# Kernel tuning notes

Hardware: AMD Instinct MI355X
Metric: run time of the kernel (lower is better)

The kernel has to match this reference:

```python
import jax, jax.numpy as jnp
import numpy as np

DIM = 256
CTX_DIM = 768
GROUPS = 8
EPS = 1e-5


def setup_inputs() -> dict:
    key = jax.random.key(0)
    ks = jax.random.split(key, 16)
    B, C, H, W, L = 16, DIM, 64, 64, 77
    s_conv = 1.0 / np.sqrt(C * 9)
    s_q = 1.0 / np.sqrt(C)
    s_kv = 1.0 / np.sqrt(CTX_DIM)
    return {
        "x": jax.random.normal(ks[0], (B, C, H, W), jnp.float32),
        "context": jax.random.normal(ks[1], (B, L, CTX_DIM), jnp.float32),
        "conv_w": jax.random.uniform(ks[2], (C, C, 3, 3), jnp.float32, -s_conv, s_conv),
        "conv_b": jax.random.uniform(ks[3], (C,), jnp.float32, -s_conv, s_conv),
        "gn_w": jnp.ones((C,), jnp.float32),
        "gn_b": jnp.zeros((C,), jnp.float32),
        "wq": jax.random.uniform(ks[4], (C, C), jnp.float32, -s_q, s_q),
        "bq": jax.random.uniform(ks[5], (C,), jnp.float32, -s_q, s_q),
        "wk": jax.random.uniform(ks[6], (C, CTX_DIM), jnp.float32, -s_kv, s_kv),
        "bk": jax.random.uniform(ks[7], (C,), jnp.float32, -s_kv, s_kv),
        "wv": jax.random.uniform(ks[8], (C, CTX_DIM), jnp.float32, -s_kv, s_kv),
        "bv": jax.random.uniform(ks[9], (C,), jnp.float32, -s_kv, s_kv),
        "wo": jax.random.uniform(ks[10], (C, C), jnp.float32, -s_q, s_q),
        "bo": jax.random.uniform(ks[11], (C,), jnp.float32, -s_q, s_q),
    }


def _group_norm(h, gn_w, gn_b):
    B, C, H, W = h.shape
    g = h.reshape(B, GROUPS, C // GROUPS, H, W)
    mean = g.mean(axis=(2, 3, 4), keepdims=True)
    var = g.var(axis=(2, 3, 4), keepdims=True)
    g = (g - mean) * jax.lax.rsqrt(var + EPS)
    h = g.reshape(B, C, H, W)
    return h * gn_w[None, :, None, None] + gn_b[None, :, None, None]


def reference(x, context, conv_w, conv_b, gn_w, gn_b, wq, bq, wk, bk, wv, bv, wo, bo):
    B, C, H, W = x.shape
    # conv 3x3, padding=1 (NCHW, OIHW)
    h = jax.lax.conv_general_dilated(
        x, conv_w, window_strides=(1, 1), padding=((1, 1), (1, 1)),
        dimension_numbers=("NCHW", "OIHW", "NCHW"))
    h = h + conv_b[None, :, None, None]
    h = jax.nn.silu(_group_norm(h, gn_w, gn_b))
    # flatten spatial -> tokens: [B, HW, C]
    hf = h.reshape(B, C, H * W).transpose(0, 2, 1)
    q = hf @ wq.T + bq                     # [B, HW, C]
    k = context @ wk.T + bk                # [B, L, C]
    v = context @ wv.T + bv                # [B, L, C]
    scale = 1.0 / jnp.sqrt(jnp.asarray(C, q.dtype))
    att = jax.nn.softmax(jnp.einsum("bqc,bkc->bqk", q, k) * scale, axis=-1)
    o = jnp.einsum("bqk,bkc->bqc", att, v) @ wo.T + bo
    h_att = o.transpose(0, 2, 1).reshape(B, C, H, W)
    return x + h_att
```

## Files before the change

### kernel.cpp

```cpp
#include <hip/hip_runtime.h>
#include <stdint.h>

#define B_  16
#define C_  256
#define HW_ 4096
#define Hp  66
#define PP  4356
#define EPS_ 1e-5f

typedef unsigned short u16;
typedef unsigned int   u32;
typedef __attribute__((ext_vector_type(4))) float  f32x4;
typedef __attribute__((ext_vector_type(8))) __bf16 bf16x8;
typedef __attribute__((ext_vector_type(8))) u16    u16x8;

__device__ __forceinline__ float bf2f(u16 u){ u32 x = ((u32)u)<<16; float f; __builtin_memcpy(&f,&x,4); return f; }
__device__ __forceinline__ u16 f2bf(float f){ u32 x; __builtin_memcpy(&x,&f,4); u32 r = x + 0x7fffu + ((x>>16)&1u); return (u16)(r>>16); }

__device__ __forceinline__ void g2l16(const void* g, void* l){
  __builtin_amdgcn_global_load_lds((__attribute__((address_space(1))) void*)(void*)g,
                                   (__attribute__((address_space(3))) void*)l, 16, 0, 0);
}
__device__ __forceinline__ bf16x8 ldfrag(const u16* p){
  u16x8 r = *(const u16x8*)p;
  return __builtin_bit_cast(bf16x8, r);
}

__global__ __launch_bounds__(256) void k_pad(const float* __restrict__ x, u16* __restrict__ xpT){
  int bid = blockIdx.x; int b = bid/66, hh = bid - b*66; int tid = threadIdx.x;
  u16* rowbase = xpT + (size_t)(b*PP + hh*Hp)*C_;
  if(hh==0 || hh==65){
    u32* p = (u32*)rowbase;
    for(int i=tid;i<66*C_/2;i+=256) p[i]=0u;
    return;
  }
  if(tid<128) ((u32*)rowbase)[tid]=0u;
  else ((u32*)(rowbase + 65*C_))[tid-128]=0u;
  int h = hh-1;
  __shared__ float Lt[64*65];
  for(int cc=0; cc<4; cc++){
    int c0=cc*64;
    int ci = tid>>2, w0 = (tid&3)*16;
    const float* xs = x + ((size_t)(b*C_ + c0+ci)*HW_) + h*64 + w0;
    for(int j=0;j<4;j++){
      float4 v = *(const float4*)(xs + j*4);
      Lt[ci*65 + w0 + j*4 + 0] = v.x;
      Lt[ci*65 + w0 + j*4 + 1] = v.y;
      Lt[ci*65 + w0 + j*4 + 2] = v.z;
      Lt[ci*65 + w0 + j*4 + 3] = v.w;
    }
    __syncthreads();
    int w = tid>>2, cj = (tid&3)*16;
    union { u16 u[16]; uint4 v[2]; } outu;
    for(int j=0;j<16;j++) outu.u[j] = f2bf(Lt[(cj+j)*65 + w]);
    uint4* dst = (uint4*)(rowbase + (size_t)(w+1)*C_ + c0 + cj);
    dst[0]=outu.v[0]; dst[1]=outu.v[1];
    __syncthreads();
  }
}

__global__ __launch_bounds__(256) void k_repack(
    const float* __restrict__ conv_w, const float* __restrict__ wq, const float* __restrict__ wo,
    const float* __restrict__ wk, const float* __restrict__ wv, const float* __restrict__ ctx,
    u16* __restrict__ wBt, u16* __restrict__ wqB, u16* __restrict__ woB,
    u16* __restrict__ wkvB, u16* __restrict__ ctxB, float* __restrict__ stats){
  int i = blockIdx.x*256 + threadIdx.x;
  if(i < 589824){ int co = i/2304, k = i - co*2304; int t = k>>8, ci = k&255;
    wBt[i] = f2bf(conv_w[(co*256+ci)*9 + t]); return; }
  i -= 589824;
  if(i < 65536){ wqB[i] = f2bf(wq[i]); return; } i -= 65536;
  if(i < 65536){ woB[i] = f2bf(wo[i]); return; } i -= 65536;
  if(i < 196608){ wkvB[i] = f2bf(wk[i]); return; } i -= 196608;
  if(i < 196608){ wkvB[196608+i] = f2bf(wv[i]); return; } i -= 196608;
  if(i < 946176){ ctxB[i] = f2bf(ctx[i]); return; } i -= 946176;
  if(i < 512){ stats[i] = 0.f; }
}

__global__ __launch_bounds__(256, 2) void k_conv(const u16* __restrict__ xpT, const u16* __restrict__ wBt,
    const float* __restrict__ conv_b, u16* __restrict__ h, float* __restrict__ stats){
  __shared__ u16 As[264*32];
  __shared__ u16 Bs[256*32];
  int bid = blockIdx.x;
  int b = bid >> 5, hp = bid & 31;
  int tid = threadIdx.x;
  int w = tid>>6, lane = tid&63, ln = lane&15, qd = lane>>4;
  int wm = w&1, wn = w>>1;
  const u16* Abase = xpT + (size_t)(b*PP + hp*132)*C_;
  f32x4 acc[4][8] = {};
  int hr_[4], wp_[4];
  #pragma unroll
  for(int mf=0;mf<4;mf++){ int p = wm*64 + mf*16 + ln; hr_[mf] = p>>6; wp_[mf] = p&63; }

  for(int ci=0; ci<8; ci++){
    int ci0 = ci*32;
    #pragma unroll
    for(int r=0;r<5;r++){
      int c = r*256 + tid;
      if(c < 1056){
        int ipix = c>>2, atom = c&3;
        g2l16(Abase + (size_t)ipix*C_ + ci0 + atom*8, &As[c*8]);
      }
    }
    for(int t=0;t<9;t++){
      int dy = (t*11)>>5, dx = t - dy*3;
      #pragma unroll
      for(int r=0;r<4;r++){
        int c = r*256 + tid;
        int co = c>>2, atom = c&3;
        g2l16(wBt + (size_t)co*2304 + t*256 + ci0 + atom*8, &Bs[c*8]);
      }
      __syncthreads();
      bf16x8 af[4], bfv[8];
      #pragma unroll
      for(int mf=0;mf<4;mf++){
        int ipix = (hr_[mf]+dy)*66 + wp_[mf] + dx;
        af[mf] = ldfrag(&As[ipix*32 + qd*8]);
      }
      #pragma unroll
      for(int nf=0;nf<8;nf++) bfv[nf] = ldfrag(&Bs[(wn*128+nf*16+ln)*32 + qd*8]);
      #pragma unroll
      for(int mf=0;mf<4;mf++)
        #pragma unroll
        for(int nf=0;nf<8;nf++)
          acc[mf][nf] = __builtin_amdgcn_mfma_f32_16x16x32_bf16(af[mf], bfv[nf], acc[mf][nf], 0,0,0);
      __syncthreads();
    }
  }
  float s[4]={0,0,0,0}, q[4]={0,0,0,0};
  int p0 = hp*128;
  for(int nf=0;nf<8;nf++){
    int n = wn*128 + nf*16 + ln;
    float bias = conv_b[n];
    for(int mf=0;mf<4;mf++){
      for(int r=0;r<4;r++){
        int p = wm*64 + mf*16 + qd*4 + r;
        float v = acc[mf][nf][r] + bias;
        h[((size_t)(b*HW_ + p0 + p))*C_ + n] = f2bf(v);
        s[nf>>1]+=v; q[nf>>1]+=v*v;
      }
    }
  }
  for(int off=32;off>=1;off>>=1){
    #pragma unroll
    for(int g=0;g<4;g++){ s[g]+=__shfl_down(s[g],off,64); q[g]+=__shfl_down(q[g],off,64); }
  }
  if(lane==0){
    #pragma unroll
    for(int g=0;g<4;g++){
      atomicAdd(&stats[(b*8 + wn*4 + g)*2+0], s[g]);
      atomicAdd(&stats[(b*8 + wn*4 + g)*2+1], q[g]);
    }
  }
}

__global__ __launch_bounds__(256) void k_gnsilu(u16* __restrict__ hbuf, const float* __restrict__ stats,
      const float* __restrict__ gnw, const float* __restrict__ gnb){
  size_t i = ((size_t)blockIdx.x*256 + threadIdx.x)*4;
  int c0 = (int)(i & 255);
  size_t row = i >> 8;
  int b = (int)(row >> 12);
  int g = c0 >> 5;
  float sm = stats[(b*8+g)*2], qm = stats[(b*8+g)*2+1];
  float mean = sm*(1.f/131072.f);
  float var  = qm*(1.f/131072.f) - mean*mean;
  float rstd = rsqrtf(var + EPS_);
  u32* p = (u32*)(hbuf + i);
  u32 v0 = p[0], v1 = p[1];
  u16 in[4] = {(u16)(v0&0xffff),(u16)(v0>>16),(u16)(v1&0xffff),(u16)(v1>>16)};
  u16 outv[4];
  for(int j=0;j<4;j++){
    float v = bf2f(in[j]);
    v = (v-mean)*rstd*gnw[c0+j] + gnb[c0+j];
    float s = v/(1.f+__expf(-v));
    outv[j] = f2bf(s);
  }
  p[0] = (u32)outv[0] | ((u32)outv[1]<<16);
  p[1] = (u32)outv[2] | ((u32)outv[3]<<16);
}

__global__ __launch_bounds__(256) void k_qproj(const u16* __restrict__ hf, const u16* __restrict__ wqB,
    const float* __restrict__ bq, u16* __restrict__ qb){
  __shared__ u16 As[128*32];
  __shared__ u16 Bs[128*32];
  int bid = blockIdx.x;
  int nt = bid & 1, mt = bid >> 1;
  int co0 = nt*128;
  int tid = threadIdx.x;
  int w=tid>>6, lane=tid&63, ln=lane&15, qd=lane>>4, wm=w>>1, wn=w&1;
  int srow=tid>>2, koff=(tid&3)*8;
  f32x4 acc[4][4] = {};
  for(int kt=0;kt<8;kt++){
    for(int j=0;j<2;j++){
      int m = srow + j*64;
      g2l16(hf  + ((size_t)(mt*128+m)*256 + kt*32 + koff), &As[(size_t)tid*8 + j*2048]);
      g2l16(wqB + ((size_t)(co0+m)*256 + kt*32 + koff),    &Bs[(size_t)tid*8 + j*2048]);
    }
    __syncthreads();
    bf16x8 af[4], bfv[4];
    for(int mf=0;mf<4;mf++) af[mf]=ldfrag(&As[(wm*64+mf*16+ln)*32+qd*8]);
    for(int nf=0;nf<4;nf++) bfv[nf]=ldfrag(&Bs[(wn*64+nf*16+ln)*32+qd*8]);
    for(int mf=0;mf<4;mf++) for(int nf=0;nf<4;nf++)
      acc[mf][nf]=__builtin_amdgcn_mfma_f32_16x16x32_bf16(af[mf],bfv[nf],acc[mf][nf],0,0,0);
    __syncthreads();
  }
  for(int mf=0;mf<4;mf++) for(int nf=0;nf<4;nf++){
    int nl=wn*64+nf*16+ln; float bias=bq[co0+nl];
    for(int r=0;r<4;r++){
      int ml=wm*64+mf*16+qd*4+r;
      qb[((size_t)(mt*128+ml))*256 + co0+nl] = f2bf(acc[mf][nf][r]+bias);
    }
  }
}

__global__ __launch_bounds__(256) void k_kvproj(const u16* __restrict__ ctxB, const u16* __restrict__ wkvB,
    const float* __restrict__ bk, const float* __restrict__ bv,
    u16* __restrict__ kb, u16* __restrict__ vT){
  __shared__ u16 As[64*128];
  __shared__ u16 Bs[64*128];
  int bid = blockIdx.x;
  int nt = bid & 7, mt = bid >> 3;
  int n0 = nt*64, m0 = mt*64;
  int tid=threadIdx.x, w=tid>>6, lane=tid&63, ln=lane&15, qd=lane>>4;
  int wm = w&1, wn = w>>1;
  f32x4 acc[2][2]={};
  for(int kt=0;kt<6;kt++){
    #pragma unroll
    for(int r=0;r<4;r++){
      int c = r*256 + tid;
      int row = c>>4, atom = c&15;
      g2l16(ctxB + ((size_t)(m0+row)*768 + kt*128 + atom*8), &As[c*8]);
      g2l16(wkvB + ((size_t)(n0+row)*768 + kt*128 + atom*8), &Bs[c*8]);
    }
    __syncthreads();
    #pragma unroll
    for(int kk=0;kk<4;kk++){
      bf16x8 af[2], bfv[2];
      #pragma unroll
      for(int mf=0;mf<2;mf++) af[mf]=ldfrag(&As[(wm*32+mf*16+ln)*128 + kk*32 + qd*8]);
      #pragma unroll
      for(int nf=0;nf<2;nf++) bfv[nf]=ldfrag(&Bs[(wn*32+nf*16+ln)*128 + kk*32 + qd*8]);
      #pragma unroll
      for(int mf=0;mf<2;mf++)
        #pragma unroll
        for(int nf=0;nf<2;nf++)
          acc[mf][nf]=__builtin_amdgcn_mfma_f32_16x16x32_bf16(af[mf],bfv[nf],acc[mf][nf],0,0,0);
    }
    __syncthreads();
  }
  for(int mf=0;mf<2;mf++) for(int nf=0;nf<2;nf++){
    int ng = n0 + wn*32 + nf*16 + ln;
    float bias = ng<256 ? bk[ng] : bv[ng-256];
    for(int r=0;r<4;r++){
      int mg = m0 + wm*32 + mf*16 + qd*4 + r;
      if(mg<1232){
        float v=acc[mf][nf][r]+bias;
        int bb=mg/77, l=mg-bb*77;
        if(ng<256) kb[((size_t)(bb*77+l))*256+ng]=f2bf(v);
        else vT[((size_t)(bb*256+(ng-256)))*96 + l]=f2bf(v);
      }
    }
  }
}

__global__ __launch_bounds__(256) void k_attn(const u16* __restrict__ qg, const u16* __restrict__ kb,
    const u16* __restrict__ vT, u16* __restrict__ ob){
  __shared__ u16 Qs[4096];
  __shared__ u16 KVs[4096];
  __shared__ u16 Sb[128*84];
  __shared__ u16 Pb[128*104];
  int bid=blockIdx.x; int b=bid>>5, qt=bid&31; int p0=qt*128;
  int tid=threadIdx.x, w=tid>>6, lane=tid&63, ln=lane&15, qd=lane>>4;
  int srow=tid>>2, koff=(tid&3)*8;
  f32x4 Sa[2][5]={};
  for(int kt=0;kt<8;kt++){
    for(int j=0;j<2;j++){
      int m=srow+j*64;
      g2l16(qg + ((size_t)(b*HW_+p0+m)*256 + kt*32+koff), &Qs[(size_t)tid*8+j*2048]);
    }
    for(int j=0;j<2;j++){
      int cja = tid + j*256;
      if(cja < 320){
        int l = cja>>2, ko2=(cja&3)*8;
        g2l16(kb + ((size_t)(b*77+l)*256 + kt*32+ko2), &KVs[(size_t)cja*8]);
      }
    }
    __syncthreads();
    bf16x8 af[2], bfv[5];
    for(int mf=0;mf<2;mf++) af[mf]=ldfrag(&Qs[(w*32+mf*16+ln)*32+qd*8]);
    for(int nf=0;nf<5;nf++) bfv[nf]=ldfrag(&KVs[(nf*16+ln)*32+qd*8]);
    for(int mf=0;mf<2;mf++) for(int nf=0;nf<5;nf++)
      Sa[mf][nf]=__builtin_amdgcn_mfma_f32_16x16x32_bf16(af[mf],bfv[nf],Sa[mf][nf],0,0,0);
    __syncthreads();
  }
  for(int mf=0;mf<2;mf++) for(int nf=0;nf<5;nf++) for(int r=0;r<4;r++){
    int ml=w*32+mf*16+qd*4+r, nl=nf*16+ln;
    Sb[ml*84+nl]=f2bf(Sa[mf][nf][r]*0.0625f);
  }
  __syncthreads();
  if(tid<128){
    const u16* srp = &Sb[tid*84];
    u16* prow = &Pb[tid*104];
    float mx=-1e30f;
    for(int j2=0;j2<77;j2++){ float v=bf2f(srp[j2]); mx=fmaxf(mx,v); }
    float sum=0.f;
    for(int j2=0;j2<77;j2++){ float e=__expf(bf2f(srp[j2])-mx); sum+=e; prow[j2]=f2bf(e); }
    float inv=1.f/sum;
    for(int j2=0;j2<77;j2++){ prow[j2]=f2bf(bf2f(prow[j2])*inv); }
    for(int j2=77;j2<104;j2++) prow[j2]=0;
  }
  __syncthreads();
  for(int nh=0;nh<2;nh++){
    f32x4 Oa[2][8]={};
    for(int kt2=0;kt2<3;kt2++){
      for(int j=0;j<2;j++){
        int chunk=tid+j*256;
        int co=chunk>>2, ko2=(chunk&3)*8;
        g2l16(vT + ((size_t)(b*256+nh*128+co)*96 + kt2*32+ko2), &KVs[(size_t)chunk*8]);
      }
      __syncthreads();
      bf16x8 af[2], bfv[8];
      for(int mf=0;mf<2;mf++) af[mf]=ldfrag(&Pb[(w*32+mf*16+ln)*104 + kt2*32+qd*8]);
      for(int nf=0;nf<8;nf++) bfv[nf]=ldfrag(&KVs[(nf*16+ln)*32+qd*8]);
      for(int mf=0;mf<2;mf++) for(int nf=0;nf<8;nf++)
        Oa[mf][nf]=__builtin_amdgcn_mfma_f32_16x16x32_bf16(af[mf],bfv[nf],Oa[mf][nf],0,0,0);
      __syncthreads();
    }
    for(int mf=0;mf<2;mf++) for(int nf=0;nf<8;nf++) for(int r=0;r<4;r++){
      int ml=w*32+mf*16+qd*4+r, nl=nh*128+nf*16+ln;
      ob[((size_t)(b*HW_+p0+ml))*256+nl]=f2bf(Oa[mf][nf][r]);
    }
  }
}

__global__ __launch_bounds__(256) void k_oproj(const u16* __restrict__ ob, const u16* __restrict__ woB,
    const float* __restrict__ bo, const float* __restrict__ x, float* __restrict__ outp){
  __shared__ u16 As[128*32];
  __shared__ u16 Bs[128*32];
  int bid=blockIdx.x;
  int b=bid>>6; int rr=bid&63; int cm=rr>>5, pt=rr&31;
  int c0=cm*128, p0=pt*128;
  int tid=threadIdx.x, w=tid>>6, lane=tid&63, ln=lane&15, qd=lane>>4, wm=w>>1, wn=w&1;
  int srow=tid>>2, koff=(tid&3)*8;
  f32x4 acc[4][4]={};
  for(int kt=0;kt<8;kt++){
    for(int j=0;j<2;j++){
      int m=srow+j*64;
      g2l16(woB + ((size_t)(c0+m)*256 + kt*32+koff),        &As[(size_t)tid*8+j*2048]);
      g2l16(ob  + ((size_t)(b*HW_+p0+m)*256 + kt*32+koff),  &Bs[(size_t)tid*8+j*2048]);
    }
    __syncthreads();
    bf16x8 af[4], bfv[4];
    for(int mf=0;mf<4;mf++) af[mf]=ldfrag(&As[(wm*64+mf*16+ln)*32+qd*8]);
    for(int nf=0;nf<4;nf++) bfv[nf]=ldfrag(&Bs[(wn*64+nf*16+ln)*32+qd*8]);
    for(int mf=0;mf<4;mf++) for(int nf=0;nf<4;nf++)
      acc[mf][nf]=__builtin_amdgcn_mfma_f32_16x16x32_bf16(af[mf],bfv[nf],acc[mf][nf],0,0,0);
    __syncthreads();
  }
  for(int mf=0;mf<4;mf++) for(int r=0;r<4;r++){
    int cl=c0+wm*64+mf*16+qd*4+r;
    float bias=bo[cl];
    for(int nf=0;nf<4;nf++){
      int pl=p0+wn*64+nf*16+ln;
      size_t idx=((size_t)(b*C_+cl))*HW_+pl;
      outp[idx]=x[idx]+acc[mf][nf][r]+bias;
    }
  }
}

extern "C" void kernel_launch(void* const* d_in, const int* in_sizes, int n_in,
                              void* d_out, int out_size, void* d_ws, size_t ws_size,
                              hipStream_t stream){
  const float* x      = (const float*)d_in[0];
  const float* ctx    = (const float*)d_in[1];
  const float* conv_w = (const float*)d_in[2];
  const float* conv_b = (const float*)d_in[3];
  const float* gnw    = (const float*)d_in[4];
  const float* gnb    = (const float*)d_in[5];
  const float* wq     = (const float*)d_in[6];
  const float* bq     = (const float*)d_in[7];
  const float* wk     = (const float*)d_in[8];
  const float* bk     = (const float*)d_in[9];
  const float* wv     = (const float*)d_in[10];
  const float* bv     = (const float*)d_in[11];
  const float* wo     = (const float*)d_in[12];
  const float* bo     = (const float*)d_in[13];
  char* ws = (char*)d_ws;
  u16* xpT  = (u16*)(ws + 0);
  u16* wBt  = (u16*)(ws + 35684352);
  u16* wqB  = (u16*)(ws + 36864000);
  u16* wkvB = (u16*)(ws + 36995072);
  u16* woB  = (u16*)(ws + 37781504);
  u16* ctxB = (u16*)(ws + 37912576);
  u16* hbuf = (u16*)(ws + 39804928);
  u16* kbv  = (u16*)(ws + 73359360);
  u16* vT   = (u16*)(ws + 73990144);
  u16* obuf = (u16*)(ws + 74776576);
  float* stats = (float*)(ws + 108331008);
  u16* qb = xpT;
  float* outp = (float*)d_out;

  k_pad   <<<1056, 256, 0, stream>>>(x, xpT);
  k_repack<<<8050, 256, 0, stream>>>(conv_w, wq, wo, wk, wv, ctx, wBt, wqB, woB, wkvB, ctxB, stats);
  k_conv  <<<512,  256, 0, stream>>>(xpT, wBt, conv_b, hbuf, stats);
  k_gnsilu<<<16384,256, 0, stream>>>(hbuf, stats, gnw, gnb);
  k_qproj <<<1024, 256, 0, stream>>>(hbuf, wqB, bq, qb);
  k_kvproj<<<160,  256, 0, stream>>>(ctxB, wkvB, bk, bv, kbv, vT);
  k_attn  <<<512,  256, 0, stream>>>(qb, kbv, vT, obuf);
  k_oproj <<<1024, 256, 0, stream>>>(obuf, woB, bo, x, outp);
}
```

Baseline: 385.3 us.

## Double-buffer conv weight tiles and XOR-swizzle LDS layout in conv kernel

The conv kernel now double-buffers the weight (B) tile in shared memory, prefetching the next tap's weights while the MFMAs for the current tap run, so one barrier per tap replaces two. Both the A and B tiles use an XOR swizzle on the 16-byte atom index to cut LDS bank conflicts on fragment reads. Global and LDS addresses are precomputed once outside the loop. The cost is an extra 16KB of LDS per block, which may limit occupancy at two blocks per CU. A-tile reloads between channel chunks still stall, though there is no check that the prefetched B data has landed before use beyond the barrier.

```diff
diff --git a/kernel.cpp b/kernel.cpp
--- a/kernel.cpp
+++ b/kernel.cpp
@@ -79,7 +79,7 @@
 __global__ __launch_bounds__(256, 2) void k_conv(const u16* __restrict__ xpT, const u16* __restrict__ wBt,
     const float* __restrict__ conv_b, u16* __restrict__ h, float* __restrict__ stats){
   __shared__ u16 As[264*32];
-  __shared__ u16 Bs[256*32];
+  __shared__ u16 Bs[2][256*32];
   int bid = blockIdx.x;
   int b = bid >> 5, hp = bid & 31;
   int tid = threadIdx.x;
@@ -90,39 +90,61 @@
   int hr_[4], wp_[4];
   #pragma unroll
   for(int mf=0;mf<4;mf++){ int p = wm*64 + mf*16 + ln; hr_[mf] = p>>6; wp_[mf] = p&63; }
-
+  int bIdx[8];
+  #pragma unroll
+  for(int nf=0;nf<8;nf++){ int n = wn*128 + nf*16 + ln; bIdx[nf] = n*32 + ((qd ^ ((n>>1)&3))<<3); }
+  const u16* aSrc[5]; int aDst[5]; bool aOk[5];
+  #pragma unroll
+  for(int r=0;r<5;r++){
+    int c = r*256 + tid;
+    aOk[r] = (c < 1056);
+    int row = c>>2, at = (c&3) ^ ((row>>1)&3);
+    aSrc[r] = Abase + (size_t)row*C_ + at*8;
+    aDst[r] = c*8;
+  }
+  const u16* bSrc[4]; int bDst[4];
+  #pragma unroll
+  for(int r=0;r<4;r++){
+    int c = r*256 + tid; int row = c>>2, at = (c&3) ^ ((row>>1)&3);
+    bSrc[r] = wBt + (size_t)row*2304 + at*8;
+    bDst[r] = c*8;
+  }
+  #pragma unroll
+  for(int r=0;r<5;r++) if(aOk[r]) g2l16(aSrc[r], &As[aDst[r]]);
+  #pragma unroll
+  for(int r=0;r<4;r++) g2l16(bSrc[r], &Bs[0][bDst[r]]);
+  __syncthreads();
+  int step = 0;
   for(int ci=0; ci<8; ci++){
-    int ci0 = ci*32;
-    #pragma unroll
-    for(int r=0;r<5;r++){
-      int c = r*256 + tid;
-      if(c < 1056){
-        int ipix = c>>2, atom = c&3;
-        g2l16(Abase + (size_t)ipix*C_ + ci0 + atom*8, &As[c*8]);
-      }
-    }
-    for(int t=0;t<9;t++){
-      int dy = (t*11)>>5, dx = t - dy*3;
-      #pragma unroll
-      for(int r=0;r<4;r++){
-        int c = r*256 + tid;
-        int co = c>>2, atom = c&3;
-        g2l16(wBt + (size_t)co*2304 + t*256 + ci0 + atom*8, &Bs[c*8]);
-      }
-      __syncthreads();
+    for(int t=0;t<9;t++,step++){
+      int cb = step&1;
+      if(step<71){
+        int tn  = (t==8) ? 0      : t+1;
+        int cin = (t==8) ? (ci+1) : ci;
+        int off = tn*256 + cin*32;
+        #pragma unroll
+        for(int r=0;r<4;r++) g2l16(bSrc[r]+off, &Bs[cb^1][bDst[r]]);
+      }
+      int dy=(t*11)>>5, dx=t-dy*3;
       bf16x8 af[4], bfv[8];
       #pragma unroll
       for(int mf=0;mf<4;mf++){
         int ipix = (hr_[mf]+dy)*66 + wp_[mf] + dx;
-        af[mf] = ldfrag(&As[ipix*32 + qd*8]);
-      }
-      #pragma unroll
-      for(int nf=0;nf<8;nf++) bfv[nf] = ldfrag(&Bs[(wn*128+nf*16+ln)*32 + qd*8]);
+        af[mf] = ldfrag(&As[ipix*32 + ((qd ^ ((ipix>>1)&3))<<3)]);
+      }
+      #pragma unroll
+      for(int nf=0;nf<8;nf++) bfv[nf] = ldfrag(&Bs[cb][bIdx[nf]]);
       #pragma unroll
       for(int mf=0;mf<4;mf++)
         #pragma unroll
         for(int nf=0;nf<8;nf++)
           acc[mf][nf] = __builtin_amdgcn_mfma_f32_16x16x32_bf16(af[mf], bfv[nf], acc[mf][nf], 0,0,0);
+      __syncthreads();
+    }
+    if(ci<7){
+      int off = (ci+1)*32;
+      #pragma unroll
+      for(int r=0;r<5;r++) if(aOk[r]) g2l16(aSrc[r]+off, &As[aDst[r]]);
       __syncthreads();
     }
   }
```

Measured after the change: 453.2 us. 17.6% more time.

## Fuse GroupNorm+SiLU into Q projection GEMM prologue with full-N tiles

Applied to the files above, without the earlier changes.

Removes the standalone GroupNorm/SiLU kernel and applies normalization and SiLU while staging the activation tile into LDS inside the Q projection GEMM. Each block now covers all 256 output channels (128x256 tile, 512 blocks), so the activation is read once and normalized once. A register prefetch of the next K-slice of h overlaps the global loads with compute. This avoids a full read-modify-write pass over the 32 MB bf16 intermediate, at the cost of more accumulator registers (launch bounds 256,2) and fewer blocks.

```diff
diff --git a/kernel.cpp b/kernel.cpp
--- a/kernel.cpp
+++ b/kernel.cpp
@@ -153,61 +153,80 @@
   }
 }
 
-__global__ __launch_bounds__(256) void k_gnsilu(u16* __restrict__ hbuf, const float* __restrict__ stats,
-      const float* __restrict__ gnw, const float* __restrict__ gnb){
-  size_t i = ((size_t)blockIdx.x*256 + threadIdx.x)*4;
-  int c0 = (int)(i & 255);
-  size_t row = i >> 8;
-  int b = (int)(row >> 12);
-  int g = c0 >> 5;
-  float sm = stats[(b*8+g)*2], qm = stats[(b*8+g)*2+1];
-  float mean = sm*(1.f/131072.f);
-  float var  = qm*(1.f/131072.f) - mean*mean;
-  float rstd = rsqrtf(var + EPS_);
-  u32* p = (u32*)(hbuf + i);
-  u32 v0 = p[0], v1 = p[1];
-  u16 in[4] = {(u16)(v0&0xffff),(u16)(v0>>16),(u16)(v1&0xffff),(u16)(v1>>16)};
-  u16 outv[4];
-  for(int j=0;j<4;j++){
-    float v = bf2f(in[j]);
-    v = (v-mean)*rstd*gnw[c0+j] + gnb[c0+j];
-    float s = v/(1.f+__expf(-v));
-    outv[j] = f2bf(s);
-  }
-  p[0] = (u32)outv[0] | ((u32)outv[1]<<16);
-  p[1] = (u32)outv[2] | ((u32)outv[3]<<16);
-}
-
-__global__ __launch_bounds__(256) void k_qproj(const u16* __restrict__ hf, const u16* __restrict__ wqB,
+__global__ __launch_bounds__(256, 2) void k_qgn(const u16* __restrict__ hbuf, const u16* __restrict__ wqB,
+    const float* __restrict__ stats, const float* __restrict__ gnw, const float* __restrict__ gnb,
     const float* __restrict__ bq, u16* __restrict__ qb){
   __shared__ u16 As[128*32];
-  __shared__ u16 Bs[128*32];
-  int bid = blockIdx.x;
-  int nt = bid & 1, mt = bid >> 1;
-  int co0 = nt*128;
+  __shared__ u16 Bs[256*32];
+  int mt = blockIdx.x;
+  int b = mt >> 5;
   int tid = threadIdx.x;
-  int w=tid>>6, lane=tid&63, ln=lane&15, qd=lane>>4, wm=w>>1, wn=w&1;
-  int srow=tid>>2, koff=(tid&3)*8;
-  f32x4 acc[4][4] = {};
-  for(int kt=0;kt<8;kt++){
-    for(int j=0;j<2;j++){
-      int m = srow + j*64;
-      g2l16(hf  + ((size_t)(mt*128+m)*256 + kt*32 + koff), &As[(size_t)tid*8 + j*2048]);
-      g2l16(wqB + ((size_t)(co0+m)*256 + kt*32 + koff),    &Bs[(size_t)tid*8 + j*2048]);
-    }
-    __syncthreads();
-    bf16x8 af[4], bfv[4];
-    for(int mf=0;mf<4;mf++) af[mf]=ldfrag(&As[(wm*64+mf*16+ln)*32+qd*8]);
-    for(int nf=0;nf<4;nf++) bfv[nf]=ldfrag(&Bs[(wn*64+nf*16+ln)*32+qd*8]);
-    for(int mf=0;mf<4;mf++) for(int nf=0;nf<4;nf++)
-      acc[mf][nf]=__builtin_amdgcn_mfma_f32_16x16x32_bf16(af[mf],bfv[nf],acc[mf][nf],0,0,0);
-    __syncthreads();
-  }
-  for(int mf=0;mf<4;mf++) for(int nf=0;nf<4;nf++){
-    int nl=wn*64+nf*16+ln; float bias=bq[co0+nl];
+  int w = tid>>6, lane = tid&63, ln = lane&15, qd = lane>>4;
+  int wm = w&1, wn = w>>1;
+  int pr = tid>>1, half = tid&1;
+  const u16* hsrc = hbuf + ((size_t)(mt*128+pr))*256 + half*16;
+  f32x4 acc[4][8] = {};
+  uint4 ra0, ra1, rb0, rb1;
+  ra0 = *(const uint4*)(hsrc);
+  ra1 = *(const uint4*)(hsrc + 8);
+  for(int kt=0; kt<8; kt++){
+    float sm = stats[(b*8+kt)*2], qm = stats[(b*8+kt)*2+1];
+    float mean = sm*(1.f/131072.f);
+    float rstd = rsqrtf(qm*(1.f/131072.f) - mean*mean + EPS_);
+    int c0 = kt*32 + half*16;
+    float4 gw0 = *(const float4*)(gnw+c0), gw1 = *(const float4*)(gnw+c0+4);
+    float4 gw2 = *(const float4*)(gnw+c0+8), gw3 = *(const float4*)(gnw+c0+12);
+    float4 gb0 = *(const float4*)(gnb+c0), gb1 = *(const float4*)(gnb+c0+4);
+    float4 gb2 = *(const float4*)(gnb+c0+8), gb3 = *(const float4*)(gnb+c0+12);
+    float gwv[16] = {gw0.x,gw0.y,gw0.z,gw0.w, gw1.x,gw1.y,gw1.z,gw1.w,
+                     gw2.x,gw2.y,gw2.z,gw2.w, gw3.x,gw3.y,gw3.z,gw3.w};
+    float gbv[16] = {gb0.x,gb0.y,gb0.z,gb0.w, gb1.x,gb1.y,gb1.z,gb1.w,
+                     gb2.x,gb2.y,gb2.z,gb2.w, gb3.x,gb3.y,gb3.z,gb3.w};
+    u16 inu[16];
+    ((uint4*)inu)[0] = ra0; ((uint4*)inu)[1] = ra1;
+    u16 outu[16];
+    #pragma unroll
+    for(int j=0;j<16;j++){
+      float v = bf2f(inu[j]);
+      v = (v-mean)*rstd*gwv[j] + gbv[j];
+      float s = v/(1.f+__expf(-v));
+      outu[j] = f2bf(s);
+    }
+    u16* adst = &As[pr*32 + half*16];
+    ((uint4*)adst)[0] = ((uint4*)outu)[0];
+    ((uint4*)adst)[1] = ((uint4*)outu)[1];
+    #pragma unroll
     for(int r=0;r<4;r++){
-      int ml=wm*64+mf*16+qd*4+r;
-      qb[((size_t)(mt*128+ml))*256 + co0+nl] = f2bf(acc[mf][nf][r]+bias);
+      int c = r*256 + tid;
+      int co = c>>2, atom = c&3;
+      g2l16(wqB + (size_t)co*256 + kt*32 + atom*8, &Bs[c*8]);
+    }
+    if(kt<7){
+      rb0 = *(const uint4*)(hsrc + (kt+1)*32);
+      rb1 = *(const uint4*)(hsrc + (kt+1)*32 + 8);
+    }
+    __syncthreads();
+    bf16x8 af[4], bfv[8];
+    #pragma unroll
+    for(int mf=0;mf<4;mf++) af[mf] = ldfrag(&As[(wm*64+mf*16+ln)*32 + qd*8]);
+    #pragma unroll
+    for(int nf=0;nf<8;nf++) bfv[nf] = ldfrag(&Bs[(wn*128+nf*16+ln)*32 + qd*8]);
+    #pragma unroll
+    for(int mf=0;mf<4;mf++)
+      #pragma unroll
+      for(int nf=0;nf<8;nf++)
+        acc[mf][nf] = __builtin_amdgcn_mfma_f32_16x16x32_bf16(af[mf], bfv[nf], acc[mf][nf], 0,0,0);
+    __syncthreads();
+    ra0 = rb0; ra1 = rb1;
+  }
+  for(int nf=0;nf<8;nf++){
+    int n = wn*128 + nf*16 + ln;
+    float bias = bq[n];
+    for(int mf=0;mf<4;mf++){
+      for(int r=0;r<4;r++){
+        int ml = wm*64 + mf*16 + qd*4 + r;
+        qb[((size_t)(mt*128+ml))*256 + n] = f2bf(acc[mf][nf][r]+bias);
+      }
     }
   }
 }
@@ -402,8 +421,7 @@
   k_pad   <<<1056, 256, 0, stream>>>(x, xpT);
   k_repack<<<8050, 256, 0, stream>>>(conv_w, wq, wo, wk, wv, ctx, wBt, wqB, woB, wkvB, ctxB, stats);
   k_conv  <<<512,  256, 0, stream>>>(xpT, wBt, conv_b, hbuf, stats);
-  k_gnsilu<<<16384,256, 0, stream>>>(hbuf, stats, gnw, gnb);
-  k_qproj <<<1024, 256, 0, stream>>>(hbuf, wqB, bq, qb);
+  k_qgn   <<<512,  256, 0, stream>>>(hbuf, wqB, stats, gnw, gnb, bq, qb);
   k_kvproj<<<160,  256, 0, stream>>>(ctxB, wkvB, bk, bv, kbv, vT);
   k_attn  <<<512,  256, 0, stream>>>(qb, kbv, vT, obuf);
   k_oproj <<<1024, 256, 0, stream>>>(obuf, woB, bo, x, outp);
```

Result: no change. 382.3 us (-0.8%).
